# Performance work log

Measured on AMD Instinct MI355X. Metric: run time of the kernel, lower is better.

The kernel has to match this reference:

```python
import jax, jax.numpy as jnp
import numpy as np

N, E, C, L, G, O = 100000, 1600000, 128, 7, 2, 40
BETA = 0.9
HEADS, HC = 1, 128  # heads=1, head_channels=hidden_channels=128


def setup_inputs() -> dict:
    key = jax.random.key(0)
    ks = jax.random.split(key, 16)
    s = 0.05  # ~ torch Linear init std for fan_in=128
    inp = {
        'x': jax.random.normal(ks[0], (N, C), jnp.float32),
        'edge_index': jax.random.randint(ks[1], (2, E), 0, N, jnp.int64),
        'Wh': jax.random.normal(ks[2], (L, C, C)) * s,
        'bh': jax.random.normal(ks[3], (L, C)) * s,
        'Wg': jax.random.normal(ks[4], (L, C, C)) * s,
        'bg': jax.random.normal(ks[5], (L, C)) * s,
        'Wl': jax.random.normal(ks[6], (L, C, C)) * s,
        'bl': jax.random.normal(ks[7], (L, C)) * s,
        'ln_g': jnp.ones((L, C)), 'ln_b': jnp.zeros((L, C)),
        'bn_g': jnp.ones((L, C)), 'bn_b': jnp.zeros((L, C)),
        'bn_rm': jnp.zeros((L, C)), 'bn_rv': jnp.ones((L, C)),
        'gWh': jax.random.normal(ks[8], (G, C, C)) * s,
        'gbh': jax.random.normal(ks[9], (G, C)) * s,
        'gWk': jax.random.normal(ks[10], (G, C, C)) * s,
        'gWv': jax.random.normal(ks[11], (G, C, C)) * s,
        'gln_g': jnp.ones((G, C)), 'gln_b': jnp.zeros((G, C)),
        'gWo': jax.random.normal(ks[12], (G, C, C)) * s,
        'gbo': jax.random.normal(ks[13], (G, C)) * s,
        'f_ln_g': jnp.ones((C,)), 'f_ln_b': jnp.zeros((C,)),
        'Wp': jax.random.normal(ks[14], (O, C)) * s,
        'bp': jax.random.normal(ks[15], (O,)) * s,
    }
    return inp


def _layer_norm(x, g, b, eps=1e-5):
    mu = jnp.mean(x, axis=-1, keepdims=True)
    var = jnp.mean((x - mu) ** 2, axis=-1, keepdims=True)
    return (x - mu) * jax.lax.rsqrt(var + eps) * g + b


def reference(x, edge_index, Wh, bh, Wg, bg, Wl, bl, ln_g, ln_b,
              bn_g, bn_b, bn_rm, bn_rv, gWh, gbh, gWk, gWv,
              gln_g, gln_b, gWo, gbo, f_ln_g, f_ln_b, Wp, bp):
    n = x.shape[0]
    src, dst = edge_index[0], edge_index[1]
    # gcn_norm with add_self_loops=True: deg over destination incl. self loop
    deg = jnp.zeros((n,), x.dtype).at[dst].add(1.0) + 1.0
    dinv = jax.lax.rsqrt(deg)
    enorm = (dinv[src] * dinv[dst])[:, None]   # [E,1]
    selfw = (dinv * dinv)[:, None]             # [N,1] self-loop weight

    x_local = jnp.zeros_like(x @ Wh[0].T)
    for i in range(L):
        h = jax.nn.relu(x @ Wh[i].T + bh[i])
        xw = x @ Wg[i].T                                  # GCN lin (bias separate)
        agg = jax.ops.segment_sum(xw[src] * enorm, dst, num_segments=n)
        conv = agg + xw * selfw + bg[i]
        x = conv + x @ Wl[i].T + bl[i]
        # BatchNorm1d in eval mode (running stats)
        x = (x - bn_rm[i]) * jax.lax.rsqrt(bn_rv[i] + 1e-5) * bn_g[i] + bn_b[i]
        x = jax.nn.relu(x)
        x = (1.0 - BETA) * _layer_norm(h * x, ln_g[i], ln_b[i]) + BETA * x
        x_local = x_local + x

    # global linear attention (PolynormerAttention, qk_shared=True, qkv_bias=False)
    xg = _layer_norm(x_local, f_ln_g, f_ln_b)
    for j in range(G):
        h = xg @ gWh[j].T + gbh[j]
        k = jax.nn.sigmoid(xg @ gWk[j].T).reshape(n, HEADS, HC)
        q = k
        v = (xg @ gWv[j].T).reshape(n, HEADS, HC)
        kv = jnp.einsum('ndh,ndm->dhm', k, v)            # [heads,hc,hc]
        num = jnp.einsum('ndh,dhm->ndm', q, kv)          # [N,heads,hc]
        k_sum = jnp.sum(k, axis=0)                       # [heads,hc]
        den = jnp.einsum('ndh,dh->nd', q, k_sum)[..., None]
        attn = (num / (den + 1e-6)).reshape(n, HEADS * HC)
        xg = _layer_norm(attn, gln_g[j], gln_b[j]) * (h + BETA)
        xg = jax.nn.relu(xg @ gWo[j].T + gbo[j])

    return xg @ Wp.T + bp
```

## Files before the change

### kernel.cpp

```cpp
#include <hip/hip_runtime.h>

typedef unsigned short u16;
typedef unsigned int u32;
typedef __attribute__((ext_vector_type(8))) short short8;
typedef __attribute__((ext_vector_type(8))) unsigned short ushort8v;
typedef __attribute__((ext_vector_type(4))) float f32x4;

#define CDIM 128

__device__ __forceinline__ float b2f(u16 u){ return __uint_as_float(((unsigned)u)<<16); }
__device__ __forceinline__ u16 f2b(float f){
  unsigned x = __float_as_uint(f);
  unsigned r = (x + 0x7fffu + ((x>>16)&1u)) >> 16;
  return (u16)r;
}
__device__ __forceinline__ float wsum64(float v){
  #pragma unroll
  for(int d=1; d<64; d<<=1) v += __shfl_xor(v, d, 64);
  return v;
}
__device__ __forceinline__ float wsum16(float v){
  v += __shfl_xor(v, 1, 64);
  v += __shfl_xor(v, 2, 64);
  v += __shfl_xor(v, 4, 64);
  v += __shfl_xor(v, 8, 64);
  return v;
}

__global__ void k_probe(const u32* __restrict__ x, const u32* __restrict__ ei, int* __restrict__ flags){
  __shared__ int s_bf, s_nz;
  if(threadIdx.x == 0){ s_bf = 0; s_nz = 0; }
  __syncthreads();
  int c_bf = 0, c_nz = 0;
  for(int i = threadIdx.x; i < 4096; i += 256){
    u32 w = x[i];
    u32 e = (w >> 7) & 0xFFu;
    if(e >= 100u && e <= 140u) c_bf++;
    if(ei[2*i + 1] != 0u) c_nz++;
  }
  atomicAdd(&s_bf, c_bf);
  atomicAdd(&s_nz, c_nz);
  __syncthreads();
  if(threadIdx.x == 0){
    flags[0] = (s_bf < 2048) ? 1 : 0;
    flags[1] = (s_nz < 8) ? 1 : 0;
  }
}

__global__ void k_cvt_x(const void* __restrict__ src, u16* __restrict__ dst, int n,
                        const int* __restrict__ flags){
  int i = (blockIdx.x*256 + threadIdx.x)*8;
  if(i + 7 >= n) return;
  if(flags[0]){
    const float* s = (const float*)src + i;
    float4 a = *(const float4*)s;
    float4 b = *(const float4*)(s + 4);
    ushort8v o;
    o[0]=f2b(a.x); o[1]=f2b(a.y); o[2]=f2b(a.z); o[3]=f2b(a.w);
    o[4]=f2b(b.x); o[5]=f2b(b.y); o[6]=f2b(b.z); o[7]=f2b(b.w);
    *(ushort8v*)(dst + i) = o;
  } else {
    *(ushort8v*)(dst + i) = *(const ushort8v*)((const u16*)src + i);
  }
}

struct CvtArgs {
  const void* src[24];
  u16* dst[24];
  int n[24];
};

__global__ void k_cvt_params(CvtArgs a, const int* __restrict__ flags){
  int seg = blockIdx.y;
  int i = blockIdx.x*256 + threadIdx.x;
  int n = a.n[seg];
  if(i >= n) return;
  if(flags[0]) a.dst[seg][i] = f2b(((const float*)a.src[seg])[i]);
  else         a.dst[seg][i] = ((const u16*)a.src[seg])[i];
}

__global__ void k_cvt_ei_count(const int* __restrict__ src, int* __restrict__ dst, int E,
                               const int* __restrict__ flags, u32* __restrict__ cnt){
  int i = blockIdx.x*256 + threadIdx.x;
  if(i >= 2*E) return;
  int v = flags[1] ? src[2*i] : src[i];
  dst[i] = v;
  if(i >= E) atomicAdd(&cnt[v], 1u);
}

__global__ __launch_bounds__(256) void k_scan1(const u32* __restrict__ cnt, int n, u32* __restrict__ bsum){
  const int lane = threadIdx.x & 63;
  const int wv = threadIdx.x >> 6;
  int i = blockIdx.x*256 + threadIdx.x;
  u32 v = (i < n) ? cnt[i] : 0u;
  #pragma unroll
  for(int d=1; d<64; d<<=1) v += (u32)__shfl_xor((int)v, d, 64);
  __shared__ u32 ws[4];
  if(lane == 0) ws[wv] = v;
  __syncthreads();
  if(threadIdx.x == 0) bsum[blockIdx.x] = ws[0] + ws[1] + ws[2] + ws[3];
}

__global__ __launch_bounds__(1024) void k_scan2(const u32* __restrict__ bsum, int nb, u32* __restrict__ bpre){
  __shared__ u32 s[1024];
  int t = threadIdx.x;
  u32 v = (t < nb) ? bsum[t] : 0u;
  s[t] = v;
  __syncthreads();
  for(int d=1; d<1024; d<<=1){
    u32 y = (t >= d) ? s[t-d] : 0u;
    __syncthreads();
    s[t] += y;
    __syncthreads();
  }
  if(t < nb) bpre[t] = s[t] - v;
}

__global__ __launch_bounds__(256) void k_scan3(const u32* __restrict__ cnt, int n,
                                               const u32* __restrict__ bpre,
                                               u32* __restrict__ rowstart, u32* __restrict__ cursor,
                                               float* __restrict__ dinv){
  const int lane = threadIdx.x & 63;
  const int wv = threadIdx.x >> 6;
  int i = blockIdx.x*256 + threadIdx.x;
  u32 v = (i < n) ? cnt[i] : 0u;
  u32 x = v;
  #pragma unroll
  for(int d=1; d<64; d<<=1){
    u32 y = (u32)__shfl_up((int)x, d, 64);
    if(lane >= d) x += y;
  }
  __shared__ u32 ws[4];
  if(lane == 63) ws[wv] = x;
  __syncthreads();
  u32 woff = 0;
  #pragma unroll
  for(int w=0; w<4; w++) if(w < wv) woff += ws[w];
  u32 incl = x + woff;
  u32 rs = bpre[blockIdx.x] + incl - v;
  if(i < n){
    rowstart[i] = rs;
    cursor[i] = rs;
    dinv[i] = rsqrtf((float)(v + 1u));
    if(i == n-1) rowstart[n] = rs + v;
  }
}

__global__ __launch_bounds__(256) void k_scatter8(
  const int* __restrict__ ei, int E, int Nn, int nsl,
  u32* __restrict__ cursor, const float* __restrict__ dinv, int2* __restrict__ colw)
{
  const int r = blockIdx.x & 7;
  const int slice = blockIdx.x >> 3;
  const int q = (Nn + 7) >> 3;
  const int lo = r*q;
  const int hi = (lo + q < Nn) ? lo + q : Nn;
  const int chunk = (E + nsl - 1) / nsl;
  int e0 = slice*chunk;
  int e1 = e0 + chunk; if(e1 > E) e1 = E;
  for(int e = e0 + threadIdx.x; e < e1; e += 256){
    int d = ei[E + e];
    if(d >= lo && d < hi){
      int s = ei[e];
      u32 p = atomicAdd(&cursor[d], 1u);
      colw[p] = make_int2(s, __float_as_int(dinv[s]));
    }
  }
}

__global__ __launch_bounds__(256) void k_gemm3(
  const u16* __restrict__ A, int M,
  const u16* __restrict__ W0, const u16* __restrict__ bs0, int op0, u16* __restrict__ O0,
  const u16* __restrict__ W1, const u16* __restrict__ bs1, int op1, u16* __restrict__ O1,
  const u16* __restrict__ W2, const u16* __restrict__ bs2, int op2, u16* __restrict__ O2)
{
  __shared__ u16 stg[4][32][72];
  const int lane = threadIdx.x & 63;
  const int wv = threadIdx.x >> 6;
  const int l16 = lane & 15, quad = lane >> 4;
  const long nbase = (long)blockIdx.x*128 + wv*32;
  u16 (*st)[72] = stg[wv];

  short8 xf[2][4];
  #pragma unroll
  for(int nt=0; nt<2; nt++){
    long r = nbase + nt*16 + l16; if(r >= M) r = M-1;
    const u16* ap = A + r*CDIM + quad*8;
    #pragma unroll
    for(int kt=0; kt<4; kt++)
      xf[nt][kt] = *(const short8*)(ap + kt*32);
  }

  const int srow = lane >> 3;
  const int schk = lane & 7;

  #pragma unroll
  for(int w=0; w<3; w++){
    const u16* Wm = (w==0) ? W0 : (w==1) ? W1 : W2;
    const u16* bp = (w==0) ? bs0 : (w==1) ? bs1 : bs2;
    const int  op = (w==0) ? op0 : (w==1) ? op1 : op2;
    u16*       Op = (w==0) ? O0 : (w==1) ? O1 : O2;
    #pragma unroll
    for(int half=0; half<2; half++){
      #pragma unroll
      for(int c2=0; c2<4; c2++){
        const int ct = half*4 + c2;
        f32x4 acc0 = {0.f,0.f,0.f,0.f}, acc1 = {0.f,0.f,0.f,0.f};
        const u16* wp = Wm + (ct*16 + l16)*CDIM + quad*8;
        #pragma unroll
        for(int kt=0; kt<4; kt++){
          short8 wf = *(const short8*)(wp + kt*32);
          acc0 = __builtin_amdgcn_mfma_f32_16x16x32_bf16(wf, xf[0][kt], acc0, 0, 0, 0);
          acc1 = __builtin_amdgcn_mfma_f32_16x16x32_bf16(wf, xf[1][kt], acc1, 0, 0, 0);
        }
        float bv[4] = {0.f,0.f,0.f,0.f};
        if(bp){
          ushort4 bq = *(const ushort4*)(bp + ct*16 + quad*4);
          bv[0]=b2f(bq.x); bv[1]=b2f(bq.y); bv[2]=b2f(bq.z); bv[3]=b2f(bq.w);
        }
        #pragma unroll
        for(int nt=0; nt<2; nt++){
          f32x4 a = nt ? acc1 : acc0;
          u16 o[4];
          #pragma unroll
          for(int g=0; g<4; g++){
            float v = a[g] + bv[g];
            if(op == 1) v = fmaxf(v, 0.f);
            else if(op == 2) v = 1.f/(1.f + __expf(-v));
            o[g] = f2b(v);
          }
          u32 p0 = (u32)o[0] | ((u32)o[1] << 16);
          u32 p1 = (u32)o[2] | ((u32)o[3] << 16);
          *(uint2*)&st[nt*16 + l16][c2*16 + quad*4] = make_uint2(p0, p1);
        }
      }
      #pragma unroll
      for(int i=0; i<4; i++){
        int row = i*8 + srow;
        long node = nbase + row;
        ushort8v v = *(const ushort8v*)&st[row][schk*8];
        if(node < M)
          *(ushort8v*)(Op + (size_t)node*CDIM + half*64 + schk*8) = v;
      }
    }
  }
}

__global__ __launch_bounds__(256) void k_layer_epi(
  const u16* __restrict__ xw, const u16* __restrict__ h, const u16* __restrict__ xl,
  const int2* __restrict__ colw, const u32* __restrict__ rowstart, const float* __restrict__ dinv,
  const u16* __restrict__ bg, const u16* __restrict__ bng, const u16* __restrict__ bnb,
  const u16* __restrict__ bnrm, const u16* __restrict__ bnrv,
  const u16* __restrict__ lng, const u16* __restrict__ lnb,
  const u16* __restrict__ flng, const u16* __restrict__ flnb,
  float* __restrict__ xlocal, u16* __restrict__ xout, int n, int first, int final)
{
  const int lane = threadIdx.x & 63;
  const int quad = lane >> 4;
  const int l16 = lane & 15;
  const int wv = threadIdx.x >> 6;
  int node = blockIdx.x*16 + wv*4 + quad;
  const int valid = (node < n);
  if(!valid) node = n - 1;
  const int cg = l16*8;
  u32 j0 = rowstart[node], j1 = rowstart[node+1];
  float a[8];
  #pragma unroll
  for(int g=0; g<8; g++) a[g] = 0.f;

  for(u32 base = j0; base < j1; base += 16){
    int cnt = (int)(j1 - base); if(cnt > 16) cnt = 16;
    int2 pw = make_int2(0, 0);
    if(l16 < cnt) pw = colw[base + l16];
    ushort8v v[16]; float w[16];
    #pragma unroll
    for(int u=0; u<16; u++){
      int s = __shfl(pw.x, quad*16 + u, 64);
      w[u] = __int_as_float(__shfl(pw.y, quad*16 + u, 64));
      v[u] = *(const ushort8v*)(xw + (size_t)s*CDIM + cg);
    }
    #pragma unroll
    for(int u=0; u<16; u++){
      #pragma unroll
      for(int g=0; g<8; g++) a[g] = fmaf(w[u], b2f(v[u][g]), a[g]);
    }
  }

  float dn = dinv[node], sw = dn*dn;
  size_t nb = (size_t)node*CDIM + cg;
  ushort8v xwv  = *(const ushort8v*)(xw + nb);
  ushort8v xlv  = *(const ushort8v*)(xl + nb);
  ushort8v hv   = *(const ushort8v*)(h  + nb);
  ushort8v bgv  = *(const ushort8v*)(bg + cg);
  ushort8v bngv = *(const ushort8v*)(bng + cg);
  ushort8v bnbv = *(const ushort8v*)(bnb + cg);
  ushort8v bnrmv= *(const ushort8v*)(bnrm + cg);
  ushort8v bnrvv= *(const ushort8v*)(bnrv + cg);
  ushort8v lngv = *(const ushort8v*)(lng + cg);
  ushort8v lnbv = *(const ushort8v*)(lnb + cg);

  float x3[8], t[8];
  float ts = 0.f;
  #pragma unroll
  for(int g=0; g<8; g++){
    float x1 = a[g]*dn + b2f(xwv[g])*sw + b2f(bgv[g]) + b2f(xlv[g]);
    float sc = rsqrtf(b2f(bnrvv[g]) + 1e-5f) * b2f(bngv[g]);
    float x2 = (x1 - b2f(bnrmv[g]))*sc + b2f(bnbv[g]);
    x3[g] = fmaxf(x2, 0.f);
    t[g] = b2f(hv[g]) * x3[g];
    ts += t[g];
  }
  float mu = wsum16(ts) * (1.f/128.f);
  float vs = 0.f;
  #pragma unroll
  for(int g=0; g<8; g++){ float d = t[g] - mu; vs = fmaf(d, d, vs); }
  float inv = rsqrtf(wsum16(vs)*(1.f/128.f) + 1e-5f);

  float xn[8], xl2[8];
  #pragma unroll
  for(int g=0; g<8; g++){
    float y = (t[g] - mu)*inv*b2f(lngv[g]) + b2f(lnbv[g]);
    xn[g] = 0.1f*y + 0.9f*x3[g];
  }
  if(first){
    #pragma unroll
    for(int g=0; g<8; g++) xl2[g] = xn[g];
  } else {
    f32x4 p0 = *(const f32x4*)(xlocal + nb);
    f32x4 p1 = *(const f32x4*)(xlocal + nb + 4);
    xl2[0]=p0[0]+xn[0]; xl2[1]=p0[1]+xn[1]; xl2[2]=p0[2]+xn[2]; xl2[3]=p0[3]+xn[3];
    xl2[4]=p1[0]+xn[4]; xl2[5]=p1[1]+xn[5]; xl2[6]=p1[2]+xn[6]; xl2[7]=p1[3]+xn[7];
  }
  if(!final){
    if(valid){
      f32x4 q0 = {xl2[0],xl2[1],xl2[2],xl2[3]};
      f32x4 q1 = {xl2[4],xl2[5],xl2[6],xl2[7]};
      *(f32x4*)(xlocal + nb)     = q0;
      *(f32x4*)(xlocal + nb + 4) = q1;
      ushort8v o;
      #pragma unroll
      for(int g=0; g<8; g++) o[g] = f2b(xn[g]);
      *(ushort8v*)(xout + nb) = o;
    }
  } else {
    float ss = 0.f;
    #pragma unroll
    for(int g=0; g<8; g++) ss += xl2[g];
    float mu2 = wsum16(ss) * (1.f/128.f);
    float v2 = 0.f;
    #pragma unroll
    for(int g=0; g<8; g++){ float e = xl2[g] - mu2; v2 = fmaf(e, e, v2); }
    float inv2 = rsqrtf(wsum16(v2)*(1.f/128.f) + 1e-5f);
    ushort8v flngv = *(const ushort8v*)(flng + cg);
    ushort8v flnbv = *(const ushort8v*)(flnb + cg);
    if(valid){
      ushort8v o;
      #pragma unroll
      for(int g=0; g<8; g++)
        o[g] = f2b((xl2[g] - mu2)*inv2*b2f(flngv[g]) + b2f(flnbv[g]));
      *(ushort8v*)(xout + nb) = o;
    }
  }
}

__global__ __launch_bounds__(256) void k_kv(
  const u16* __restrict__ kk, const u16* __restrict__ vv, int n, int npb,
  float* __restrict__ part)
{
  __shared__ float sk[8][128];
  __shared__ float sv[8][128];
  const int tid = threadIdx.x;
  const int tr = tid >> 4, tc = tid & 15;
  float acc[8][8];
  #pragma unroll
  for(int i=0;i<8;i++){
    #pragma unroll
    for(int j=0;j<8;j++) acc[i][j] = 0.f;
  }
  float ks[8];
  #pragma unroll
  for(int i=0;i<8;i++) ks[i] = 0.f;
  int start = blockIdx.x * npb;
  int end = start + npb; if(end > n) end = n;
  const int lr = tid >> 5;
  const int lc = (tid & 31) * 4;
  for(int g0 = start; g0 < end; g0 += 8){
    int cnt = end - g0; if(cnt > 8) cnt = 8;
    __syncthreads();
    if(lr < cnt){
      ushort4 kq = *(const ushort4*)(kk + (size_t)(g0+lr)*CDIM + lc);
      ushort4 vq = *(const ushort4*)(vv + (size_t)(g0+lr)*CDIM + lc);
      sk[lr][lc] = b2f(kq.x); sk[lr][lc+1] = b2f(kq.y); sk[lr][lc+2] = b2f(kq.z); sk[lr][lc+3] = b2f(kq.w);
      sv[lr][lc] = b2f(vq.x); sv[lr][lc+1] = b2f(vq.y); sv[lr][lc+2] = b2f(vq.z); sv[lr][lc+3] = b2f(vq.w);
    }
    __syncthreads();
    for(int r=0; r<cnt; r++){
      float4 ka = *(const float4*)&sk[r][tr*8];
      float4 kb = *(const float4*)&sk[r][tr*8+4];
      float4 va = *(const float4*)&sv[r][tc*8];
      float4 vb = *(const float4*)&sv[r][tc*8+4];
      float kr[8] = {ka.x,ka.y,ka.z,ka.w,kb.x,kb.y,kb.z,kb.w};
      float vr[8] = {va.x,va.y,va.z,va.w,vb.x,vb.y,vb.z,vb.w};
      #pragma unroll
      for(int i=0;i<8;i++){
        #pragma unroll
        for(int j=0;j<8;j++) acc[i][j] = fmaf(kr[i], vr[j], acc[i][j]);
      }
      if(tc == 0){
        #pragma unroll
        for(int i=0;i<8;i++) ks[i] += kr[i];
      }
    }
  }
  float* p = part + (size_t)blockIdx.x * 16512;
  #pragma unroll
  for(int i=0;i<8;i++){
    #pragma unroll
    for(int j=0;j<8;j++)
      p[(size_t)(tc*8+j)*CDIM + tr*8 + i] = acc[i][j];
  }
  if(tc == 0){
    #pragma unroll
    for(int i=0;i<8;i++) p[16384 + tr*8 + i] = ks[i];
  }
}

__global__ void k_kvred(const float* __restrict__ part, int nb, u16* __restrict__ Bext){
  int i = blockIdx.x*256 + threadIdx.x;
  if(i >= 144*128) return;
  float s = 0.f;
  if(i < 16512){
    #pragma unroll 8
    for(int b=0;b<nb;b++) s += part[(size_t)b*16512 + i];
  }
  Bext[i] = f2b(s);
}

__global__ __launch_bounds__(256) void k_attn(
  const u16* __restrict__ q, const u16* __restrict__ Bext, const u16* __restrict__ hg,
  const u16* __restrict__ g, const u16* __restrict__ b,
  const u16* __restrict__ Wo, const u16* __restrict__ bo,
  const u16* __restrict__ Wp, const u16* __restrict__ bp,
  u16* __restrict__ xgout, void* __restrict__ outv,
  int M, int last, const int* __restrict__ flags)
{
  __shared__ u16 stg[4][32*136];
  const int lane = threadIdx.x & 63;
  const int wv = threadIdx.x >> 6;
  const int l16 = lane & 15, quad = lane >> 4;
  const long rbase = (long)blockIdx.x*128 + wv*32;
  u16* st = stg[wv];

  {
    short8 af[2][4];
    #pragma unroll
    for(int rt=0; rt<2; rt++){
      long r = rbase + rt*16 + l16; if(r >= M) r = M-1;
      const u16* ap = q + r*CDIM + quad*8;
      #pragma unroll
      for(int kt=0; kt<4; kt++)
        af[rt][kt] = *(const short8*)(ap + kt*32);
    }
    f32x4 acc[2][9];
    f32x4 zero = {0.f,0.f,0.f,0.f};
    #pragma unroll
    for(int rt=0; rt<2; rt++){
      #pragma unroll
      for(int ct=0; ct<9; ct++) acc[rt][ct] = zero;
    }
    #pragma unroll
    for(int ct=0; ct<9; ct++){
      const u16* wp = Bext + (ct*16 + l16)*CDIM + quad*8;
      #pragma unroll
      for(int kt=0; kt<4; kt++){
        short8 bf = *(const short8*)(wp + kt*32);
        acc[0][ct] = __builtin_amdgcn_mfma_f32_16x16x32_bf16(af[0][kt], bf, acc[0][ct], 0, 0, 0);
        acc[1][ct] = __builtin_amdgcn_mfma_f32_16x16x32_bf16(af[1][kt], bf, acc[1][ct], 0, 0, 0);
      }
    }
    #pragma unroll
    for(int rt=0; rt<2; rt++){
      float rden[4];
      #pragma unroll
      for(int gi=0; gi<4; gi++){
        float dv = __shfl(acc[rt][8][gi], lane & 48, 64);
        rden[gi] = 1.f/(dv + 1e-6f);
      }
      #pragma unroll
      for(int gi=0; gi<4; gi++){
        float sum = 0.f;
        #pragma unroll
        for(int ct=0; ct<8; ct++) sum += acc[rt][ct][gi]*rden[gi];
        float mu = wsum16(sum) * (1.f/128.f);
        float vs = 0.f;
        #pragma unroll
        for(int ct=0; ct<8; ct++){ float d = acc[rt][ct][gi]*rden[gi] - mu; vs = fmaf(d, d, vs); }
        float inv = rsqrtf(wsum16(vs)*(1.f/128.f) + 1e-5f);
        const int rowl = rt*16 + quad*4 + gi;
        #pragma unroll
        for(int ct=0; ct<8; ct++){
          int col = ct*16 + l16;
          float y = (acc[rt][ct][gi]*rden[gi] - mu)*inv*b2f(g[col]) + b2f(b[col]);
          st[rowl*136 + col] = f2b(y);
        }
      }
    }
  }
  #pragma unroll
  for(int p2=0; p2<8; p2++){
    int row = (p2>>2)*16 + (lane>>2);
    int seg = (lane&3) + (p2&3)*4;
    long node = rbase + row;
    if(node >= M) node = M-1;
    ushort8v yv = *(const ushort8v*)&st[row*136 + seg*8];
    ushort8v hv = *(const ushort8v*)(hg + (size_t)node*CDIM + seg*8);
    ushort8v o;
    #pragma unroll
    for(int i2=0; i2<8; i2++)
      o[i2] = f2b(b2f(yv[i2]) * (b2f(hv[i2]) + 0.9f));
    *(ushort8v*)&st[row*136 + seg*8] = o;
  }
  short8 pf[2][4];
  #pragma unroll
  for(int nt=0; nt<2; nt++){
    #pragma unroll
    for(int kt=0; kt<4; kt++)
      pf[nt][kt] = *(const short8*)&st[(nt*16 + l16)*136 + quad*8 + kt*32];
  }
  #pragma unroll
  for(int ct=0; ct<8; ct++){
    f32x4 a0 = {0.f,0.f,0.f,0.f}, a1 = {0.f,0.f,0.f,0.f};
    const u16* wp = Wo + (ct*16 + l16)*CDIM + quad*8;
    #pragma unroll
    for(int kt=0; kt<4; kt++){
      short8 wf = *(const short8*)(wp + kt*32);
      a0 = __builtin_amdgcn_mfma_f32_16x16x32_bf16(wf, pf[0][kt], a0, 0, 0, 0);
      a1 = __builtin_amdgcn_mfma_f32_16x16x32_bf16(wf, pf[1][kt], a1, 0, 0, 0);
    }
    ushort4 bq = *(const ushort4*)(bo + ct*16 + quad*4);
    float bv[4] = {b2f(bq.x), b2f(bq.y), b2f(bq.z), b2f(bq.w)};
    #pragma unroll
    for(int nt=0; nt<2; nt++){
      f32x4 a = nt ? a1 : a0;
      u16 o[4];
      #pragma unroll
      for(int g2=0; g2<4; g2++)
        o[g2] = f2b(fmaxf(a[g2] + bv[g2], 0.f));
      u32 p0 = (u32)o[0] | ((u32)o[1] << 16);
      u32 p1 = (u32)o[2] | ((u32)o[3] << 16);
      *(uint2*)&st[(nt*16 + l16)*136 + ct*16 + quad*4] = make_uint2(p0, p1);
    }
  }
  if(!last){
    #pragma unroll
    for(int p2=0; p2<8; p2++){
      int row = (p2>>2)*16 + (lane>>2);
      int seg = (lane&3) + (p2&3)*4;
      long node = rbase + row;
      ushort8v v = *(const ushort8v*)&st[row*136 + seg*8];
      if(node < M)
        *(ushort8v*)(xgout + (size_t)node*CDIM + seg*8) = v;
    }
  } else {
    const int f32m = flags[0];
    short8 pf2[2][4];
    #pragma unroll
    for(int nt=0; nt<2; nt++){
      #pragma unroll
      for(int kt=0; kt<4; kt++)
        pf2[nt][kt] = *(const short8*)&st[(nt*16 + l16)*136 + quad*8 + kt*32];
    }
    #pragma unroll
    for(int ct=0; ct<3; ct++){
      f32x4 a0 = {0.f,0.f,0.f,0.f}, a1 = {0.f,0.f,0.f,0.f};
      int wrow = ct*16 + l16; if(wrow > 39) wrow = 39;
      const u16* wp = Wp + wrow*CDIM + quad*8;
      #pragma unroll
      for(int kt=0; kt<4; kt++){
        short8 wf = *(const short8*)(wp + kt*32);
        a0 = __builtin_amdgcn_mfma_f32_16x16x32_bf16(wf, pf2[0][kt], a0, 0, 0, 0);
        a1 = __builtin_amdgcn_mfma_f32_16x16x32_bf16(wf, pf2[1][kt], a1, 0, 0, 0);
      }
      const int ch0 = ct*16 + quad*4;
      if(ch0 < 40){
        ushort4 bq = *(const ushort4*)(bp + ch0);
        float bv[4] = {b2f(bq.x), b2f(bq.y), b2f(bq.z), b2f(bq.w)};
        #pragma unroll
        for(int nt=0; nt<2; nt++){
          long node = rbase + nt*16 + l16;
          if(node < M){
            f32x4 a = nt ? a1 : a0;
            if(f32m){
              float* op = (float*)outv + node*40 + ch0;
              #pragma unroll
              for(int g2=0; g2<4; g2++) op[g2] = a[g2] + bv[g2];
            } else {
              u16 o[4];
              #pragma unroll
              for(int g2=0; g2<4; g2++) o[g2] = f2b(a[g2] + bv[g2]);
              u32 p0 = (u32)o[0] | ((u32)o[1] << 16);
              u32 p1 = (u32)o[2] | ((u32)o[3] << 16);
              *(uint2*)((u16*)outv + node*40 + ch0) = make_uint2(p0, p1);
            }
          }
        }
      }
    }
  }
}

extern "C" void kernel_launch(void* const* d_in, const int* in_sizes, int n_in,
                              void* d_out, int out_size, void* d_ws, size_t ws_size,
                              hipStream_t stream)
{
  (void)n_in;
  const int C = CDIM;
  const int Nn = in_sizes[0] / C;
  const int E  = in_sizes[1] / 2;

  char* ws = (char*)d_ws;
  size_t off = 0;
  auto alloc = [&](size_t bytes) -> char* {
    char* p = ws + off;
    off = (off + bytes + 255) & ~(size_t)255;
    return p;
  };
  u16*   x_cur  = (u16*)  alloc((size_t)Nn*C*2);
  float* xlocal = (float*)alloc((size_t)Nn*C*4);
  u16*   hb     = (u16*)  alloc((size_t)Nn*C*2);
  u16*   xwb    = (u16*)  alloc((size_t)Nn*C*2);
  u16*   xlb    = (u16*)  alloc((size_t)Nn*C*2);
  float* dinv   = (float*)alloc((size_t)Nn*4);
  u32*   cnt    = (u32*)  alloc((size_t)Nn*4);
  u32*   rowst  = (u32*)  alloc((size_t)(Nn+1)*4);
  u32*   cursor = (u32*)  alloc((size_t)Nn*4);
  int2*  colw   = (int2*) alloc((size_t)E*8);
  u16*   Bext   = (u16*)  alloc((size_t)144*128*2);
  int*   flags  = (int*)  alloc(256);
  u32*   bsum   = (u32*)  alloc(1024*4);
  u32*   bpre   = (u32*)  alloc(1024*4);
  size_t ptot = 0;
  for(int k=2;k<26;k++) ptot += (size_t)in_sizes[k];
  u16* pbuf = (u16*)alloc(ptot*2);

  if(off > ws_size){
    hipMemsetAsync(d_out, 0, (size_t)out_size*2, stream);
    return;
  }

  const u16* pp[26];
  {
    size_t po = 0;
    for(int k=2;k<26;k++){ pp[k] = pbuf + po; po += (size_t)in_sizes[k]; }
  }
  const u16* cWh  = pp[2];  const u16* cbh  = pp[3];
  const u16* cWg  = pp[4];  const u16* cbg  = pp[5];
  const u16* cWl  = pp[6];  const u16* cbl  = pp[7];
  const u16* clng = pp[8];  const u16* clnb = pp[9];
  const u16* cbng = pp[10]; const u16* cbnb = pp[11];
  const u16* cbnrm= pp[12]; const u16* cbnrv= pp[13];
  const u16* cgWh = pp[14]; const u16* cgbh = pp[15];
  const u16* cgWk = pp[16]; const u16* cgWv = pp[17];
  const u16* cglng= pp[18]; const u16* cglnb= pp[19];
  const u16* cgWo = pp[20]; const u16* cgbo = pp[21];
  const u16* cflng= pp[22]; const u16* cflnb= pp[23];
  const u16* cWp  = pp[24]; const u16* cbp  = pp[25];

  u16* xb  = (u16*)xlocal;
  int* eib = (int*)((char*)xlocal + (size_t)Nn*C*2);
  u16* xg  = x_cur;
  float* kvpart = xlocal;

  const int NB_KV = 512;
  const int npb = (Nn + NB_KV - 1) / NB_KV;
  const int gblk = (Nn + 127) / 128;
  const int nodeblk = (Nn + 15) / 16;
  const int nscan = (Nn + 255) / 256;
  const int NSL = 512;

  k_probe<<<1, 256, 0, stream>>>((const u32*)d_in[0], (const u32*)d_in[1], flags);
  hipMemsetAsync(cnt, 0, (size_t)Nn*4, stream);
  k_cvt_ei_count<<<(2*E + 255)/256, 256, 0, stream>>>((const int*)d_in[1], eib, E, flags, cnt);
  k_cvt_x<<<(Nn*C/8 + 255)/256, 256, 0, stream>>>(d_in[0], xb, Nn*C, flags);
  {
    CvtArgs a;
    int maxn = 0;
    for(int k=2;k<26;k++){
      a.src[k-2] = d_in[k];
      a.dst[k-2] = (u16*)pp[k];
      a.n[k-2]   = in_sizes[k];
      if(in_sizes[k] > maxn) maxn = in_sizes[k];
    }
    dim3 g((maxn + 255)/256, 24);
    k_cvt_params<<<g, 256, 0, stream>>>(a, flags);
  }

  k_scan1<<<nscan, 256, 0, stream>>>(cnt, Nn, bsum);
  k_scan2<<<1, 1024, 0, stream>>>(bsum, nscan, bpre);
  k_scan3<<<nscan, 256, 0, stream>>>(cnt, Nn, bpre, rowst, cursor, dinv);
  k_scatter8<<<NSL*8, 256, 0, stream>>>(eib, E, Nn, NSL, cursor, dinv, colw);

  const u16* xa = xb;
  for(int i=0; i<7; i++){
    k_gemm3<<<gblk, 256, 0, stream>>>(xa, Nn,
        cWh + (size_t)i*C*C, cbh + (size_t)i*C, 1, hb,
        cWg + (size_t)i*C*C, (const u16*)nullptr, 0, xwb,
        cWl + (size_t)i*C*C, cbl + (size_t)i*C, 0, xlb);
    k_layer_epi<<<nodeblk, 256, 0, stream>>>(xwb, hb, xlb, colw, rowst, dinv,
        cbg + (size_t)i*C, cbng + (size_t)i*C, cbnb + (size_t)i*C,
        cbnrm + (size_t)i*C, cbnrv + (size_t)i*C,
        clng + (size_t)i*C, clnb + (size_t)i*C,
        cflng, cflnb,
        xlocal, x_cur, Nn, (i==0) ? 1 : 0, (i==6) ? 1 : 0);
    xa = x_cur;
  }

  for(int j=0; j<2; j++){
    k_gemm3<<<gblk, 256, 0, stream>>>(xg, Nn,
        cgWh + (size_t)j*C*C, cgbh + (size_t)j*C, 0, hb,
        cgWk + (size_t)j*C*C, (const u16*)nullptr, 2, xwb,
        cgWv + (size_t)j*C*C, (const u16*)nullptr, 0, xlb);
    k_kv   <<<NB_KV, 256, 0, stream>>>(xwb, xlb, Nn, npb, kvpart);
    k_kvred<<<(144*128 + 255)/256, 256, 0, stream>>>(kvpart, NB_KV, Bext);
    k_attn <<<gblk, 256, 0, stream>>>(xwb, Bext, hb,
        cglng + (size_t)j*C, cglnb + (size_t)j*C,
        cgWo + (size_t)j*C*C, cgbo + (size_t)j*C,
        cWp, cbp, xg, d_out, Nn, (j==1) ? 1 : 0, flags);
  }
}
```

Baseline: 1.689 ms.

## Degree-sort nodes for aggregation, split gemm3 weights across grid, prefetch edge lists

Builds a degree-bucketed permutation of nodes (histogram, scan, atomic scatter) so that each wavefront in the layer epilogue handles nodes of similar in-degree, reducing divergence from mixed-length neighbor loops. The three-matrix GEMM kernel is split so each weight matrix runs in its own blockIdx.y slice, tripling the grid to raise parallelism at the cost of loading the activation tile three times. The edge-list loop also prefetches the next 16 column/weight pairs before processing the current batch. The permutation scatters node writes, which may reduce output locality.

After: 2.248 ms. +33.1%, slower.

```diff
diff --git a/kernel.cpp b/kernel.cpp
--- a/kernel.cpp
+++ b/kernel.cpp
@@ -143,6 +143,36 @@
     cursor[i] = rs;
     dinv[i] = rsqrtf((float)(v + 1u));
     if(i == n-1) rowstart[n] = rs + v;
+  }
+}
+
+__global__ void k_dhist(const u32* __restrict__ cnt, int n, u32* __restrict__ dbin){
+  int i = blockIdx.x*256 + threadIdx.x;
+  if(i < n){
+    u32 b = cnt[i]; if(b > 63u) b = 63u;
+    atomicAdd(&dbin[b], 1u);
+  }
+}
+
+__global__ __launch_bounds__(64) void k_dscan(const u32* __restrict__ dbin, u32* __restrict__ dcur){
+  int t = threadIdx.x;
+  u32 v = dbin[t];
+  u32 x = v;
+  #pragma unroll
+  for(int d=1; d<64; d<<=1){
+    u32 y = (u32)__shfl_up((int)x, d, 64);
+    if(t >= d) x += y;
+  }
+  dcur[t] = x - v;
+}
+
+__global__ void k_dperm(const u32* __restrict__ cnt, int n, u32* __restrict__ dcur,
+                        u32* __restrict__ perm){
+  int i = blockIdx.x*256 + threadIdx.x;
+  if(i < n){
+    u32 b = cnt[i]; if(b > 63u) b = 63u;
+    u32 p = atomicAdd(&dcur[b], 1u);
+    perm[p] = (u32)i;
   }
 }
 
@@ -181,6 +211,12 @@
   const long nbase = (long)blockIdx.x*128 + wv*32;
   u16 (*st)[72] = stg[wv];
 
+  const int w = blockIdx.y;
+  const u16* Wm = (w==0) ? W0 : (w==1) ? W1 : W2;
+  const u16* bp = (w==0) ? bs0 : (w==1) ? bs1 : bs2;
+  const int  op = (w==0) ? op0 : (w==1) ? op1 : op2;
+  u16*       Op = (w==0) ? O0 : (w==1) ? O1 : O2;
+
   short8 xf[2][4];
   #pragma unroll
   for(int nt=0; nt<2; nt++){
@@ -195,53 +231,46 @@
   const int schk = lane & 7;
 
   #pragma unroll
-  for(int w=0; w<3; w++){
-    const u16* Wm = (w==0) ? W0 : (w==1) ? W1 : W2;
-    const u16* bp = (w==0) ? bs0 : (w==1) ? bs1 : bs2;
-    const int  op = (w==0) ? op0 : (w==1) ? op1 : op2;
-    u16*       Op = (w==0) ? O0 : (w==1) ? O1 : O2;
-    #pragma unroll
-    for(int half=0; half<2; half++){
-      #pragma unroll
-      for(int c2=0; c2<4; c2++){
-        const int ct = half*4 + c2;
-        f32x4 acc0 = {0.f,0.f,0.f,0.f}, acc1 = {0.f,0.f,0.f,0.f};
-        const u16* wp = Wm + (ct*16 + l16)*CDIM + quad*8;
+  for(int half=0; half<2; half++){
+    #pragma unroll
+    for(int c2=0; c2<4; c2++){
+      const int ct = half*4 + c2;
+      f32x4 acc0 = {0.f,0.f,0.f,0.f}, acc1 = {0.f,0.f,0.f,0.f};
+      const u16* wp = Wm + (ct*16 + l16)*CDIM + quad*8;
+      #pragma unroll
+      for(int kt=0; kt<4; kt++){
+        short8 wf = *(const short8*)(wp + kt*32);
+        acc0 = __builtin_amdgcn_mfma_f32_16x16x32_bf16(wf, xf[0][kt], acc0, 0, 0, 0);
+        acc1 = __builtin_amdgcn_mfma_f32_16x16x32_bf16(wf, xf[1][kt], acc1, 0, 0, 0);
+      }
+      float bv[4] = {0.f,0.f,0.f,0.f};
+      if(bp){
+        ushort4 bq = *(const ushort4*)(bp + ct*16 + quad*4);
+        bv[0]=b2f(bq.x); bv[1]=b2f(bq.y); bv[2]=b2f(bq.z); bv[3]=b2f(bq.w);
+      }
+      #pragma unroll
+      for(int nt=0; nt<2; nt++){
+        f32x4 a = nt ? acc1 : acc0;
+        u16 o[4];
         #pragma unroll
-        for(int kt=0; kt<4; kt++){
-          short8 wf = *(const short8*)(wp + kt*32);
-          acc0 = __builtin_amdgcn_mfma_f32_16x16x32_bf16(wf, xf[0][kt], acc0, 0, 0, 0);
-          acc1 = __builtin_amdgcn_mfma_f32_16x16x32_bf16(wf, xf[1][kt], acc1, 0, 0, 0);
+        for(int g=0; g<4; g++){
+          float v = a[g] + bv[g];
+          if(op == 1) v = fmaxf(v, 0.f);
+          else if(op == 2) v = 1.f/(1.f + __expf(-v));
+          o[g] = f2b(v);
         }
-        float bv[4] = {0.f,0.f,0.f,0.f};
-        if(bp){
-          ushort4 bq = *(const ushort4*)(bp + ct*16 + quad*4);
-          bv[0]=b2f(bq.x); bv[1]=b2f(bq.y); bv[2]=b2f(bq.z); bv[3]=b2f(bq.w);
-        }
-        #pragma unroll
-        for(int nt=0; nt<2; nt++){
-          f32x4 a = nt ? acc1 : acc0;
-          u16 o[4];
-          #pragma unroll
-          for(int g=0; g<4; g++){
-            float v = a[g] + bv[g];
-            if(op == 1) v = fmaxf(v, 0.f);
-            else if(op == 2) v = 1.f/(1.f + __expf(-v));
-            o[g] = f2b(v);
-          }
-          u32 p0 = (u32)o[0] | ((u32)o[1] << 16);
-          u32 p1 = (u32)o[2] | ((u32)o[3] << 16);
-          *(uint2*)&st[nt*16 + l16][c2*16 + quad*4] = make_uint2(p0, p1);
-        }
-      }
-      #pragma unroll
-      for(int i=0; i<4; i++){
-        int row = i*8 + srow;
-        long node = nbase + row;
-        ushort8v v = *(const ushort8v*)&st[row][schk*8];
-        if(node < M)
-          *(ushort8v*)(Op + (size_t)node*CDIM + half*64 + schk*8) = v;
-      }
+        u32 p0 = (u32)o[0] | ((u32)o[1] << 16);
+        u32 p1 = (u32)o[2] | ((u32)o[3] << 16);
+        *(uint2*)&st[nt*16 + l16][c2*16 + quad*4] = make_uint2(p0, p1);
+      }
+    }
+    #pragma unroll
+    for(int i=0; i<4; i++){
+      int row = i*8 + srow;
+      long node = nbase + row;
+      ushort8v v = *(const ushort8v*)&st[row][schk*8];
+      if(node < M)
+        *(ushort8v*)(Op + (size_t)node*CDIM + half*64 + schk*8) = v;
     }
   }
 }
@@ -249,6 +278,7 @@
 __global__ __launch_bounds__(256) void k_layer_epi(
   const u16* __restrict__ xw, const u16* __restrict__ h, const u16* __restrict__ xl,
   const int2* __restrict__ colw, const u32* __restrict__ rowstart, const float* __restrict__ dinv,
+  const u32* __restrict__ perm,
   const u16* __restrict__ bg, const u16* __restrict__ bng, const u16* __restrict__ bnb,
   const u16* __restrict__ bnrm, const u16* __restrict__ bnrv,
   const u16* __restrict__ lng, const u16* __restrict__ lnb,
@@ -259,19 +289,21 @@
   const int quad = lane >> 4;
   const int l16 = lane & 15;
   const int wv = threadIdx.x >> 6;
-  int node = blockIdx.x*16 + wv*4 + quad;
-  const int valid = (node < n);
-  if(!valid) node = n - 1;
+  int idx = blockIdx.x*16 + wv*4 + quad;
+  const int valid = (idx < n);
+  int node = (int)perm[valid ? idx : (n-1)];
   const int cg = l16*8;
   u32 j0 = rowstart[node], j1 = rowstart[node+1];
   float a[8];
   #pragma unroll
   for(int g=0; g<8; g++) a[g] = 0.f;
 
+  int2 pw = make_int2(0, 0);
+  if(j0 < j1 && l16 < (int)(j1 - j0)) pw = colw[j0 + l16];
   for(u32 base = j0; base < j1; base += 16){
-    int cnt = (int)(j1 - base); if(cnt > 16) cnt = 16;
-    int2 pw = make_int2(0, 0);
-    if(l16 < cnt) pw = colw[base + l16];
+    int2 pwn = make_int2(0, 0);
+    u32 nb2 = base + 16;
+    if(nb2 < j1 && l16 < (int)(j1 - nb2)) pwn = colw[nb2 + l16];
     ushort8v v[16]; float w[16];
     #pragma unroll
     for(int u=0; u<16; u++){
@@ -284,6 +316,7 @@
       #pragma unroll
       for(int g=0; g<8; g++) a[g] = fmaf(w[u], b2f(v[u][g]), a[g]);
     }
+    pw = pwn;
   }
 
   float dn = dinv[node], sw = dn*dn;
@@ -634,11 +667,14 @@
   u32*   cnt    = (u32*)  alloc((size_t)Nn*4);
   u32*   rowst  = (u32*)  alloc((size_t)(Nn+1)*4);
   u32*   cursor = (u32*)  alloc((size_t)Nn*4);
+  u32*   perm   = (u32*)  alloc((size_t)Nn*4);
   int2*  colw   = (int2*) alloc((size_t)E*8);
   u16*   Bext   = (u16*)  alloc((size_t)144*128*2);
   int*   flags  = (int*)  alloc(256);
   u32*   bsum   = (u32*)  alloc(1024*4);
   u32*   bpre   = (u32*)  alloc(1024*4);
+  u32*   dbin   = (u32*)  alloc(256);
+  u32*   dcur   = (u32*)  alloc(256);
   size_t ptot = 0;
   for(int k=2;k<26;k++) ptot += (size_t)in_sizes[k];
   u16* pbuf = (u16*)alloc(ptot*2);
@@ -676,10 +712,12 @@
   const int gblk = (Nn + 127) / 128;
   const int nodeblk = (Nn + 15) / 16;
   const int nscan = (Nn + 255) / 256;
+  const int nblk256 = (Nn + 255) / 256;
   const int NSL = 512;
 
   k_probe<<<1, 256, 0, stream>>>((const u32*)d_in[0], (const u32*)d_in[1], flags);
   hipMemsetAsync(cnt, 0, (size_t)Nn*4, stream);
+  hipMemsetAsync(dbin, 0, 256, stream);
   k_cvt_ei_count<<<(2*E + 255)/256, 256, 0, stream>>>((const int*)d_in[1], eib, E, flags, cnt);
   k_cvt_x<<<(Nn*C/8 + 255)/256, 256, 0, stream>>>(d_in[0], xb, Nn*C, flags);
   {
@@ -698,15 +736,18 @@
   k_scan1<<<nscan, 256, 0, stream>>>(cnt, Nn, bsum);
   k_scan2<<<1, 1024, 0, stream>>>(bsum, nscan, bpre);
   k_scan3<<<nscan, 256, 0, stream>>>(cnt, Nn, bpre, rowst, cursor, dinv);
+  k_dhist<<<nblk256, 256, 0, stream>>>(cnt, Nn, dbin);
+  k_dscan<<<1, 64, 0, stream>>>(dbin, dcur);
+  k_dperm<<<nblk256, 256, 0, stream>>>(cnt, Nn, dcur, perm);
   k_scatter8<<<NSL*8, 256, 0, stream>>>(eib, E, Nn, NSL, cursor, dinv, colw);
 
   const u16* xa = xb;
   for(int i=0; i<7; i++){
-    k_gemm3<<<gblk, 256, 0, stream>>>(xa, Nn,
+    k_gemm3<<<dim3(gblk,3), 256, 0, stream>>>(xa, Nn,
         cWh + (size_t)i*C*C, cbh + (size_t)i*C, 1, hb,
         cWg + (size_t)i*C*C, (const u16*)nullptr, 0, xwb,
         cWl + (size_t)i*C*C, cbl + (size_t)i*C, 0, xlb);
-    k_layer_epi<<<nodeblk, 256, 0, stream>>>(xwb, hb, xlb, colw, rowst, dinv,
+    k_layer_epi<<<nodeblk, 256, 0, stream>>>(xwb, hb, xlb, colw, rowst, dinv, perm,
         cbg + (size_t)i*C, cbng + (size_t)i*C, cbnb + (size_t)i*C,
         cbnrm + (size_t)i*C, cbnrv + (size_t)i*C,
         clng + (size_t)i*C, clnb + (size_t)i*C,
@@ -716,7 +757,7 @@
   }
 
   for(int j=0; j<2; j++){
-    k_gemm3<<<gblk, 256, 0, stream>>>(xg, Nn,
+    k_gemm3<<<dim3(gblk,3), 256, 0, stream>>>(xg, Nn,
         cgWh + (size_t)j*C*C, cgbh + (size_t)j*C, 0, hb,
         cgWk + (size_t)j*C*C, (const u16*)nullptr, 2, xwb,
         cgWv + (size_t)j*C*C, (const u16*)nullptr, 0, xlb);
```

## Split fused triple GEMM across weight matrices via grid y, two row tiles per block

Applied to the files above, without the earlier changes.

The three-weight GEMM kernel now assigns each weight matrix to a separate blockIdx.y. Each block handles two 128-row tiles, one from each half of the node range, and prefetches both A tiles up front. This increases block-level parallelism and overlaps the load of the second tile with compute on the first. In exchange, each A row is read three times across blocks instead of once, and register pressure rises from holding two tiles of A fragments.

After: 1.718 ms. About the same (+1.7%).

```diff
diff --git a/kernel.cpp b/kernel.cpp
--- a/kernel.cpp
+++ b/kernel.cpp
@@ -169,7 +169,7 @@
 }
 
 __global__ __launch_bounds__(256) void k_gemm3(
-  const u16* __restrict__ A, int M,
+  const u16* __restrict__ A, int M, int hblk,
   const u16* __restrict__ W0, const u16* __restrict__ bs0, int op0, u16* __restrict__ O0,
   const u16* __restrict__ W1, const u16* __restrict__ bs1, int op1, u16* __restrict__ O1,
   const u16* __restrict__ W2, const u16* __restrict__ bs2, int op2, u16* __restrict__ O2)
@@ -178,28 +178,40 @@
   const int lane = threadIdx.x & 63;
   const int wv = threadIdx.x >> 6;
   const int l16 = lane & 15, quad = lane >> 4;
-  const long nbase = (long)blockIdx.x*128 + wv*32;
   u16 (*st)[72] = stg[wv];
 
+  const int w = blockIdx.y;
+  const u16* Wm = (w==0) ? W0 : (w==1) ? W1 : W2;
+  const u16* bp = (w==0) ? bs0 : (w==1) ? bs1 : bs2;
+  const int  op = (w==0) ? op0 : (w==1) ? op1 : op2;
+  u16*       Op = (w==0) ? O0 : (w==1) ? O1 : O2;
+
+  const long nb0 = (long)blockIdx.x*128 + wv*32;
+  const long nb1 = (long)(blockIdx.x + hblk)*128 + wv*32;
+
+  const int srow = lane >> 3;
+  const int schk = lane & 7;
+
   short8 xf[2][4];
   #pragma unroll
   for(int nt=0; nt<2; nt++){
-    long r = nbase + nt*16 + l16; if(r >= M) r = M-1;
+    long r = nb0 + nt*16 + l16; if(r >= M) r = M-1;
     const u16* ap = A + r*CDIM + quad*8;
     #pragma unroll
     for(int kt=0; kt<4; kt++)
       xf[nt][kt] = *(const short8*)(ap + kt*32);
   }
-
-  const int srow = lane >> 3;
-  const int schk = lane & 7;
-
-  #pragma unroll
-  for(int w=0; w<3; w++){
-    const u16* Wm = (w==0) ? W0 : (w==1) ? W1 : W2;
-    const u16* bp = (w==0) ? bs0 : (w==1) ? bs1 : bs2;
-    const int  op = (w==0) ? op0 : (w==1) ? op1 : op2;
-    u16*       Op = (w==0) ? O0 : (w==1) ? O1 : O2;
+  short8 xp[2][4];
+  #pragma unroll
+  for(int nt=0; nt<2; nt++){
+    long r = nb1 + nt*16 + l16; if(r >= M) r = M-1;
+    const u16* ap = A + r*CDIM + quad*8;
+    #pragma unroll
+    for(int kt=0; kt<4; kt++)
+      xp[nt][kt] = *(const short8*)(ap + kt*32);
+  }
+
+  auto process = [&](const short8 (&xa)[2][4], long nbase){
     #pragma unroll
     for(int half=0; half<2; half++){
       #pragma unroll
@@ -210,8 +222,8 @@
         #pragma unroll
         for(int kt=0; kt<4; kt++){
           short8 wf = *(const short8*)(wp + kt*32);
-          acc0 = __builtin_amdgcn_mfma_f32_16x16x32_bf16(wf, xf[0][kt], acc0, 0, 0, 0);
-          acc1 = __builtin_amdgcn_mfma_f32_16x16x32_bf16(wf, xf[1][kt], acc1, 0, 0, 0);
+          acc0 = __builtin_amdgcn_mfma_f32_16x16x32_bf16(wf, xa[0][kt], acc0, 0, 0, 0);
+          acc1 = __builtin_amdgcn_mfma_f32_16x16x32_bf16(wf, xa[1][kt], acc1, 0, 0, 0);
         }
         float bv[4] = {0.f,0.f,0.f,0.f};
         if(bp){
@@ -243,7 +255,10 @@
           *(ushort8v*)(Op + (size_t)node*CDIM + half*64 + schk*8) = v;
       }
     }
-  }
+  };
+
+  process(xf, nb0);
+  process(xp, nb1);
 }
 
 __global__ __launch_bounds__(256) void k_layer_epi(
@@ -674,6 +689,8 @@
   const int NB_KV = 512;
   const int npb = (Nn + NB_KV - 1) / NB_KV;
   const int gblk = (Nn + 127) / 128;
+  const int tiles = (Nn + 127) / 128;
+  const int hblk = (tiles + 1) / 2;
   const int nodeblk = (Nn + 15) / 16;
   const int nscan = (Nn + 255) / 256;
   const int NSL = 512;
@@ -702,7 +719,7 @@
 
   const u16* xa = xb;
   for(int i=0; i<7; i++){
-    k_gemm3<<<gblk, 256, 0, stream>>>(xa, Nn,
+    k_gemm3<<<dim3(hblk,3), 256, 0, stream>>>(xa, Nn, hblk,
         cWh + (size_t)i*C*C, cbh + (size_t)i*C, 1, hb,
         cWg + (size_t)i*C*C, (const u16*)nullptr, 0, xwb,
         cWl + (size_t)i*C*C, cbl + (size_t)i*C, 0, xlb);
@@ -716,7 +733,7 @@
   }
 
   for(int j=0; j<2; j++){
-    k_gemm3<<<gblk, 256, 0, stream>>>(xg, Nn,
+    k_gemm3<<<dim3(hblk,3), 256, 0, stream>>>(xg, Nn, hblk,
         cgWh + (size_t)j*C*C, cgbh + (size_t)j*C, 0, hb,
         cgWk + (size_t)j*C*C, (const u16*)nullptr, 2, xwb,
         cgWv + (size_t)j*C*C, (const u16*)nullptr, 0, xlb);
```
